# Optimization experiments

Hardware: AMD Instinct MI355X
Metric: run time of the kernel (lower is better)

## Reference

```python
import jax, jax.numpy as jnp
import numpy as np

HIDDEN = 4096
N_HEADS = 32
N_KV_HEADS = 8
HEAD_DIM = 128
N_GROUPS = N_HEADS // N_KV_HEADS
ROPE_THETA = 10000.0
QMAX = 127.0
B, S = 1, 2048


def setup_inputs() -> dict:
    key = jax.random.key(0)
    ks = jax.random.split(key, 5)
    hidden_states = jax.random.normal(ks[0], (B, S, HIDDEN), dtype=jnp.float32)
    # additive causal mask (Llama style: 0 on/below diagonal, large negative above)
    tril = jnp.tril(jnp.ones((S, S), dtype=bool))
    attention_mask = jnp.where(tril, 0.0, -1e9).astype(jnp.float32)[None, None]
    position_ids = jnp.arange(S, dtype=jnp.int64 if jax.config.jax_enable_x64 else jnp.int32)[None].astype(jnp.int32)
    sc = 1.0 / np.sqrt(HIDDEN)
    wq = jax.random.normal(ks[1], (HIDDEN, N_HEADS * HEAD_DIM), dtype=jnp.float32) * sc
    wk = jax.random.normal(ks[2], (HIDDEN, N_KV_HEADS * HEAD_DIM), dtype=jnp.float32) * sc
    wv = jax.random.normal(ks[3], (HIDDEN, N_KV_HEADS * HEAD_DIM), dtype=jnp.float32) * sc
    wo = jax.random.normal(ks[4], (N_HEADS * HEAD_DIM, HIDDEN), dtype=jnp.float32) * sc
    return {"hidden_states": hidden_states, "attention_mask": attention_mask,
            "position_ids": position_ids, "wq": wq, "wk": wk, "wv": wv, "wo": wo}


def _rope_cos_sin(position_ids):
    # [B, S, HEAD_DIM]
    inv_freq = 1.0 / (ROPE_THETA ** (jnp.arange(0, HEAD_DIM, 2, dtype=jnp.float32) / HEAD_DIM))
    freqs = position_ids.astype(jnp.float32)[..., None] * inv_freq  # [B,S,HEAD_DIM//2]
    emb = jnp.concatenate([freqs, freqs], axis=-1)
    return jnp.cos(emb), jnp.sin(emb)


def _rotate_half(x):
    x1, x2 = jnp.split(x, 2, axis=-1)
    return jnp.concatenate([-x2, x1], axis=-1)


def _fake_quant(x):
    scale = jnp.max(jnp.abs(x)) / QMAX  # global absmax
    return jnp.round(x / scale) * scale


def reference(hidden_states, attention_mask, position_ids, wq, wk, wv, wo):
    bsz, q_len, _ = hidden_states.shape
    q = (hidden_states @ wq).reshape(bsz, q_len, N_HEADS, HEAD_DIM).transpose(0, 2, 1, 3)
    k = (hidden_states @ wk).reshape(bsz, q_len, N_KV_HEADS, HEAD_DIM).transpose(0, 2, 1, 3)
    v = (hidden_states @ wv).reshape(bsz, q_len, N_KV_HEADS, HEAD_DIM).transpose(0, 2, 1, 3)

    cos, sin = _rope_cos_sin(position_ids)  # [B,S,D]
    cos, sin = cos[:, None], sin[:, None]   # broadcast over heads
    q = q * cos + _rotate_half(q) * sin
    k = k * cos + _rotate_half(k) * sin

    # repeat_kv: [B, Hkv, S, D] -> [B, H, S, D]
    k = jnp.repeat(k, N_GROUPS, axis=1)
    v = jnp.repeat(v, N_GROUPS, axis=1)

    # fake quant: global absmax round-trip on Q, K, V
    q = _fake_quant(q)
    k = _fake_quant(k)
    v = _fake_quant(v)

    scores = jnp.einsum('bhqd,bhkd->bhqk', q, k) / np.sqrt(HEAD_DIM)
    scores = scores + attention_mask
    probs = jax.nn.softmax(scores.astype(jnp.float32), axis=-1).astype(q.dtype)
    attn = jnp.einsum('bhqk,bhkd->bhqd', probs, v)
    attn = attn.transpose(0, 2, 1, 3).reshape(bsz, q_len, N_HEADS * HEAD_DIM)
    return attn @ wo
```

## Files before the change

kernel.cpp:

```cpp
#include <hip/hip_runtime.h>
#include <math.h>

#define S_LEN 2048
#define HID 4096
#define NH 32
#define NKV 8
#define HD 128
#define NQKV 6144

typedef __bf16 bf16x8 __attribute__((ext_vector_type(8)));
typedef float f32x4 __attribute__((ext_vector_type(4)));
typedef short short8v __attribute__((ext_vector_type(8)));

__device__ inline short f2bf(float f) {
  union { float f; unsigned u; } a; a.f = f;
  unsigned r = a.u + 0x7fffu + ((a.u >> 16) & 1u);
  return (short)(r >> 16);
}

__device__ inline void glds16(const void* g, void* l) {
  __builtin_amdgcn_global_load_lds((const __attribute__((address_space(1))) void*)g,
                                   (__attribute__((address_space(3))) void*)l, 16, 0, 0);
}

template <int CTRL>
__device__ inline float dpp_max_step(float x) {
  int y = __builtin_amdgcn_update_dpp(0, __float_as_int(x), CTRL, 0xf, 0xf, false);
  return fmaxf(x, __int_as_float(y));
}

__global__ __launch_bounds__(256) void cast_h(const float* __restrict__ X,
                                              short* __restrict__ Y, int n4) {
  int i = blockIdx.x * 256 + threadIdx.x;
  if (i >= n4) return;
  float4 v = ((const float4*)X)[i];
  short4 o;
  o.x = f2bf(v.x); o.y = f2bf(v.y); o.z = f2bf(v.z); o.w = f2bf(v.w);
  ((short4*)Y)[i] = o;
}

__global__ __launch_bounds__(256) void cast_wt(const float* __restrict__ W,
                                               short* __restrict__ Wt, int Ncols) {
  __shared__ float t[32][33];
  int n0 = blockIdx.x * 32, k0 = blockIdx.y * 32;
  int tx = threadIdx.x, ty = threadIdx.y;
  for (int j = 0; j < 4; j++)
    t[ty + 8 * j][tx] = W[(size_t)(k0 + ty + 8 * j) * Ncols + n0 + tx];
  __syncthreads();
  for (int j = 0; j < 4; j++)
    Wt[(size_t)(n0 + ty + 8 * j) * 4096 + k0 + tx] = f2bf(t[tx][ty + 8 * j]);
}

__global__ void rope_table(const int* __restrict__ pos_ids, float* __restrict__ tc,
                           float* __restrict__ ts) {
  int p = blockIdx.x, i = threadIdx.x;
  float pos = (float)pos_ids[p];
  float inv = powf(10000.0f, -((float)(2 * i)) * (1.0f / 128.0f));
  float a = pos * inv;
  tc[p * 64 + i] = cosf(a);
  ts[p * 64 + i] = sinf(a);
}

__global__ __launch_bounds__(256) void rope_absmax(float* __restrict__ C,
                                                   const float* __restrict__ tc,
                                                   const float* __restrict__ ts,
                                                   unsigned* __restrict__ scal) {
  __shared__ float lc[64], lsn[64];
  __shared__ float red[3][4];
  const int p = blockIdx.x, t = threadIdx.x;
  if (t < 64) { lc[t] = tc[p * 64 + t]; lsn[t] = ts[p * 64 + t]; }
  __syncthreads();
  float* row = C + (size_t)p * NQKV;
  float mq = 0.f, mk = 0.f, mv = 0.f;
#pragma unroll
  for (int j = 0; j < 8; j++) {
    int idx = t + 256 * j;
    int i = idx & 63, col = (idx >> 6) * 128 + i;
    float c = lc[i], s = lsn[i];
    float x1 = row[col], x2 = row[col + 64];
    float y1 = x1 * c - x2 * s, y2 = x2 * c + x1 * s;
    row[col] = y1; row[col + 64] = y2;
    mq = fmaxf(mq, fmaxf(fabsf(y1), fabsf(y2)));
  }
#pragma unroll
  for (int j = 0; j < 2; j++) {
    int idx = t + 256 * j;
    int i = idx & 63, col = 4096 + (idx >> 6) * 128 + i;
    float c = lc[i], s = lsn[i];
    float x1 = row[col], x2 = row[col + 64];
    float y1 = x1 * c - x2 * s, y2 = x2 * c + x1 * s;
    row[col] = y1; row[col + 64] = y2;
    mk = fmaxf(mk, fmaxf(fabsf(y1), fabsf(y2)));
  }
#pragma unroll
  for (int j = 0; j < 4; j++) {
    float v = row[5120 + t + 256 * j];
    mv = fmaxf(mv, fabsf(v));
  }
  for (int off = 32; off; off >>= 1) {
    mq = fmaxf(mq, __shfl_xor(mq, off, 64));
    mk = fmaxf(mk, __shfl_xor(mk, off, 64));
    mv = fmaxf(mv, __shfl_xor(mv, off, 64));
  }
  const int wave = t >> 6;
  if ((t & 63) == 0) { red[0][wave] = mq; red[1][wave] = mk; red[2][wave] = mv; }
  __syncthreads();
  if (t < 3) {
    float m = fmaxf(fmaxf(red[t][0], red[t][1]), fmaxf(red[t][2], red[t][3]));
    atomicMax(scal + t, __float_as_uint(m));
  }
}

__global__ __launch_bounds__(256) void quant_q(const float* __restrict__ C,
                                               const unsigned* __restrict__ scal,
                                               short* __restrict__ Qi) {
  int idx = blockIdx.x * 256 + threadIdx.x;
  float scale = __uint_as_float(scal[0]) * (1.0f / 127.0f);
  int p = idx >> 12, c = idx & 4095;
  Qi[idx] = f2bf(rintf(C[(size_t)p * NQKV + c] / scale));
}

__global__ __launch_bounds__(256) void quant_k(const float* __restrict__ C,
                                               const unsigned* __restrict__ scal,
                                               short* __restrict__ Ki) {
  int idx = blockIdx.x * 256 + threadIdx.x;
  float scale = __uint_as_float(scal[1]) * (1.0f / 127.0f);
  int h = idx >> 18, p = (idx >> 7) & 2047, d = idx & 127;
  Ki[idx] = f2bf(rintf(C[(size_t)p * NQKV + 4096 + h * 128 + d] / scale));
}

__global__ __launch_bounds__(256) void quant_vt(const float* __restrict__ C,
                                                const unsigned* __restrict__ scal,
                                                short* __restrict__ Vt) {
  __shared__ float t[64][65];
  int h = blockIdx.x, pt = blockIdx.y, dt = blockIdx.z;
  float scale = __uint_as_float(scal[2]) * (1.0f / 127.0f);
  int tid = threadIdx.x;
  for (int j = 0; j < 16; j++) {
    int q = tid + 256 * j;
    int pl = q >> 6, dl = q & 63;
    t[dl][pl] = C[(size_t)(pt * 64 + pl) * NQKV + 5120 + h * 128 + dt * 64 + dl];
  }
  __syncthreads();
  for (int j = 0; j < 16; j++) {
    int q = tid + 256 * j;
    int dl = q >> 6, pl = q & 63;
    Vt[(size_t)(h * 128 + dt * 64 + dl) * 2048 + pt * 64 + pl] =
        f2bf(rintf(t[dl][pl] / scale));
  }
}

__global__ __launch_bounds__(256, 2) void gemm_bt(const short* __restrict__ A, int lda,
                                                  const short* __restrict__ B,
                                                  float* __restrict__ C, int ldc, int K) {
  __shared__ alignas(16) short As[2][4096];
  __shared__ alignas(16) short Bs[2][4096];
  const int tid = threadIdx.x;
  const int wave = tid >> 6, lane = tid & 63;
  const int quad = lane >> 4, l15 = lane & 15;
  const int m0 = blockIdx.y * 128, n0 = blockIdx.x * 128;
  const int wm = (wave >> 1) * 64, wn = (wave & 1) * 64;
  f32x4 acc[4][4] = {};
  const int sr = wave * 16 + (lane >> 2);
  const int sg = (lane & 3) * 8;
  const short* Ag0 = A + (size_t)(m0 + sr) * lda + sg;
  const short* Ag1 = A + (size_t)(m0 + 64 + sr) * lda + sg;
  const short* Bg0 = B + (size_t)(n0 + sr) * K + sg;
  const short* Bg1 = B + (size_t)(n0 + 64 + sr) * K + sg;
  auto stage = [&](int kk, int b) {
    glds16(Ag0 + kk, &As[b][wave * 512]);
    glds16(Ag1 + kk, &As[b][2048 + wave * 512]);
    glds16(Bg0 + kk, &Bs[b][wave * 512]);
    glds16(Bg1 + kk, &Bs[b][2048 + wave * 512]);
  };
  stage(0, 0);
  int b = 0;
  for (int k0 = 0; k0 < K; k0 += 32) {
    __syncthreads();
    const int nk = (k0 + 32 < K) ? k0 + 32 : k0;
    stage(nk, b ^ 1);
    bf16x8 af[4], bfr[4];
#pragma unroll
    for (int t = 0; t < 4; t++) {
      af[t] = *(const bf16x8*)&As[b][(wm + t * 16 + l15) * 32 + quad * 8];
      bfr[t] = *(const bf16x8*)&Bs[b][(wn + t * 16 + l15) * 32 + quad * 8];
    }
#pragma unroll
    for (int tm = 0; tm < 4; tm++)
#pragma unroll
      for (int tn = 0; tn < 4; tn++)
        acc[tm][tn] =
            __builtin_amdgcn_mfma_f32_16x16x32_bf16(af[tm], bfr[tn], acc[tm][tn], 0, 0, 0);
    b ^= 1;
  }
#pragma unroll
  for (int tm = 0; tm < 4; tm++)
#pragma unroll
    for (int tn = 0; tn < 4; tn++) {
      const int row = m0 + wm + tm * 16 + quad * 4;
      const int col = n0 + wn + tn * 16 + l15;
#pragma unroll
      for (int r = 0; r < 4; r++) C[(size_t)(row + r) * ldc + col] = acc[tm][tn][r];
    }
}

__global__ __launch_bounds__(512, 2) void gemm_bt8(const short* __restrict__ A, int lda,
                                                   const short* __restrict__ B, int ldb,
                                                   float* __restrict__ C, int ldc, int K) {
  __shared__ alignas(16) short As[2][16384];
  __shared__ alignas(16) short Bs[2][16384];
  const int tid = threadIdx.x;
  const int wave = tid >> 6, lane = tid & 63;
  const int quad = lane >> 4, l15 = lane & 15;
  const int wm = wave >> 2, wn = wave & 3;
  const int m0 = blockIdx.y * 256, n0 = blockIdx.x * 256;

  const int rsub = lane >> 3;
  const int csw = (lane & 7) ^ rsub;
  size_t asrc[4], bsrc[4];
#pragma unroll
  for (int s = 0; s < 4; s++) {
    int row = s * 64 + wave * 8 + rsub;
    asrc[s] = (size_t)(m0 + row) * lda + csw * 8;
    bsrc[s] = (size_t)(n0 + row) * ldb + csw * 8;
  }
  const int nt = K >> 6;

  auto stA = [&](int t2) {
    const int kk = (t2 < nt ? t2 : nt - 1) << 6;
#pragma unroll
    for (int s = 0; s < 4; s++)
      glds16(A + asrc[s] + kk, &As[t2 & 1][(s * 64 + wave * 8) * 64]);
  };
  auto stB = [&](int t2) {
    const int kk = (t2 < nt ? t2 : nt - 1) << 6;
#pragma unroll
    for (int s = 0; s < 4; s++)
      glds16(B + bsrc[s] + kk, &Bs[t2 & 1][(s * 64 + wave * 8) * 64]);
  };

  int swq[2];
#pragma unroll
  for (int kc = 0; kc < 2; kc++)
    swq[kc] = l15 * 64 + (((kc * 4 + quad) ^ (l15 & 7)) * 8);

  f32x4 acc[8][4] = {};

  stB(0); stA(0);
  stB(1);
  asm volatile("s_waitcnt vmcnt(4)" ::: "memory");
  __builtin_amdgcn_s_barrier();

  for (int t = 0; t < nt; t++) {
    const short* Ab = As[t & 1];
    const short* Bb = Bs[t & 1];
    stA(t + 1);
    bf16x8 bfr[4][2];
#pragma unroll
    for (int n = 0; n < 4; n++) {
      bfr[n][0] = *(const bf16x8*)&Bb[(wn * 64 + n * 16) * 64 + swq[0]];
      bfr[n][1] = *(const bf16x8*)&Bb[(wn * 64 + n * 16) * 64 + swq[1]];
    }
    asm volatile("s_waitcnt lgkmcnt(0)" ::: "memory");
    __builtin_amdgcn_sched_barrier(0);
    __builtin_amdgcn_s_barrier();
    stB(t + 2);
    __builtin_amdgcn_s_setprio(1);
#pragma unroll
    for (int m = 0; m < 8; m++) {
      bf16x8 a0 = *(const bf16x8*)&Ab[(wm * 128 + m * 16) * 64 + swq[0]];
      bf16x8 a1 = *(const bf16x8*)&Ab[(wm * 128 + m * 16) * 64 + swq[1]];
#pragma unroll
      for (int n = 0; n < 4; n++) {
        acc[m][n] = __builtin_amdgcn_mfma_f32_16x16x32_bf16(a0, bfr[n][0], acc[m][n], 0, 0, 0);
        acc[m][n] = __builtin_amdgcn_mfma_f32_16x16x32_bf16(a1, bfr[n][1], acc[m][n], 0, 0, 0);
      }
    }
    __builtin_amdgcn_s_setprio(0);
    asm volatile("s_waitcnt vmcnt(4)" ::: "memory");
    __builtin_amdgcn_s_barrier();
    __builtin_amdgcn_sched_barrier(0);
  }
#pragma unroll
  for (int m = 0; m < 8; m++)
#pragma unroll
    for (int n = 0; n < 4; n++) {
      const int row = m0 + wm * 128 + m * 16 + quad * 4;
      const int col = n0 + wn * 64 + n * 16 + l15;
#pragma unroll
      for (int r = 0; r < 4; r++) C[(size_t)(row + r) * ldc + col] = acc[m][n][r];
    }
}

__global__ __launch_bounds__(256, 2) void attn_fused(const short* __restrict__ Qi,
                                                     const short* __restrict__ Ki,
                                                     const short* __restrict__ Vt,
                                                     const unsigned* __restrict__ scal,
                                                     short* __restrict__ Oa) {
  __shared__ alignas(16) short Ks[2][64 * 128];
  __shared__ alignas(16) short Vs[2][128 * 64];
  __shared__ alignas(16) short Ps[4][16 * 72];
  const int tid = threadIdx.x;
  const int wave = tid >> 6, lane = tid & 63;
  const int quad = lane >> 4, l15 = lane & 15;
  const int swz = l15 & 7;
  const int h = blockIdx.x & 31, pq = blockIdx.x >> 5;
  const int kvh = h >> 2;
  const float qs = __uint_as_float(scal[0]) * (1.0f / 127.0f);
  const float ksc = __uint_as_float(scal[1]) * (1.0f / 127.0f);
  const float vsc = __uint_as_float(scal[2]) * (1.0f / 127.0f);
  const float sscale = qs * ksc * 0.08838834764831845f * 1.4426950408889634f;
  const short* Kg = Ki + (size_t)kvh * S_LEN * HD;
  const short* Vg = Vt + (size_t)kvh * HD * S_LEN;

  union { short8v s; bf16x8 b; } uone;
  uone.s = short8v{0x3F80, 0x3F80, 0x3F80, 0x3F80, 0x3F80, 0x3F80, 0x3F80, 0x3F80};
  const bf16x8 vone = uone.b;

  int koff[4], voff[4];
#pragma unroll
  for (int j = 0; j < 4; j++) {
    int slot = j * 256 + tid;
    int r = slot >> 4, seg = slot & 15;
    koff[j] = r * 128 + ((seg ^ (r & 7)) * 8);
    int vr = slot >> 3, vseg = slot & 7;
    voff[j] = vr * 2048 + ((vseg ^ (vr & 7)) * 8);
  }
  auto stage = [&](int k0, int b) {
#pragma unroll
    for (int j = 0; j < 4; j++)
      glds16(Kg + (size_t)k0 * HD + koff[j], &Ks[b][(j * 256 + wave * 64) * 8]);
#pragma unroll
    for (int j = 0; j < 4; j++)
      glds16(Vg + (size_t)k0 + voff[j], &Vs[b][(j * 256 + wave * 64) * 8]);
  };

  stage(0, 0);
  int buf = 0;
  for (int ph = 0; ph < 2; ph++) {
    const int qt = ph ? 31 - pq : pq;
    const int rw = qt * 64 + wave * 16;
    bf16x8 aq[4];
#pragma unroll
    for (int kc = 0; kc < 4; kc++)
      aq[kc] = *(const bf16x8*)(Qi + (size_t)(rw + l15) * 4096 + h * 128 + kc * 32 +
                                quad * 8);
    f32x4 o[9] = {};
    float m_[4] = {-INFINITY, -INFINITY, -INFINITY, -INFINITY};
    const int nkt = qt + 1;
    for (int kt = 0; kt < nkt; kt++) {
      const int k0 = kt * 64;
      __syncthreads();
      const int nx = (kt + 1 < nkt) ? k0 + 64 : 0;
      stage(nx, buf ^ 1);

      const short* Kb = Ks[buf];
      const short* Vb = Vs[buf];
      f32x4 sf[4];
      __builtin_amdgcn_s_setprio(1);
#pragma unroll
      for (int tn = 0; tn < 4; tn++) {
        f32x4 s = {0.f, 0.f, 0.f, 0.f};
#pragma unroll
        for (int kc = 0; kc < 4; kc++) {
          bf16x8 bk = *(const bf16x8*)&Kb[(tn * 16 + l15) * 128 + ((kc * 4 + quad) ^ swz) * 8];
          s = __builtin_amdgcn_mfma_f32_16x16x32_bf16(aq[kc], bk, s, 0, 0, 0);
        }
        sf[tn] = s;
      }
      __builtin_amdgcn_s_setprio(0);

      const bool diag = (kt == qt);
#pragma unroll
      for (int r = 0; r < 4; r++) {
        const int grow = rw + quad * 4 + r;
        float mx = -3.0e38f;
        if (diag) {
#pragma unroll
          for (int tn = 0; tn < 4; tn++) {
            float v = sf[tn][r] * sscale;
            if (k0 + tn * 16 + l15 > grow) v = -3.0e38f;
            sf[tn][r] = v;
            mx = fmaxf(mx, v);
          }
        } else {
#pragma unroll
          for (int tn = 0; tn < 4; tn++) {
            float v = sf[tn][r] * sscale;
            sf[tn][r] = v;
            mx = fmaxf(mx, v);
          }
        }
        mx = dpp_max_step<0x121>(mx);
        mx = dpp_max_step<0x122>(mx);
        mx = dpp_max_step<0x124>(mx);
        mx = dpp_max_step<0x128>(mx);
        const float mo = m_[r];
        const float mn = fmaxf(mo, mx);
        m_[r] = mn;
        const float alpha = __builtin_amdgcn_exp2f(mo - mn);
#pragma unroll
        for (int tn = 0; tn < 4; tn++) {
          float p = __builtin_amdgcn_exp2f(sf[tn][r] - mn);
          Ps[wave][(quad * 4 + r) * 72 + tn * 16 + l15] =
              (short)((__float_as_uint(p) + 0x8000u) >> 16);
        }
        if (__ballot(alpha != 1.0f)) {
#pragma unroll
          for (int t = 0; t < 9; t++) o[t][r] *= alpha;
        }
      }
      __builtin_amdgcn_s_setprio(1);
#pragma unroll
      for (int kk = 0; kk < 2; kk++) {
        bf16x8 ap = *(const bf16x8*)&Ps[wave][l15 * 72 + kk * 32 + quad * 8];
#pragma unroll
        for (int tn = 0; tn < 8; tn++) {
          bf16x8 bv = *(const bf16x8*)&Vb[(tn * 16 + l15) * 64 + ((kk * 4 + quad) ^ swz) * 8];
          o[tn] = __builtin_amdgcn_mfma_f32_16x16x32_bf16(ap, bv, o[tn], 0, 0, 0);
        }
        o[8] = __builtin_amdgcn_mfma_f32_16x16x32_bf16(ap, vone, o[8], 0, 0, 0);
      }
      __builtin_amdgcn_s_setprio(0);
      buf ^= 1;
    }
#pragma unroll
    for (int r = 0; r < 4; r++) {
      const int grow = rw + quad * 4 + r;
      const float sc = vsc / o[8][r];
#pragma unroll
      for (int tn = 0; tn < 8; tn++)
        Oa[(size_t)grow * 4096 + h * 128 + tn * 16 + l15] = f2bf(o[tn][r] * sc);
    }
  }
}

extern "C" void kernel_launch(void* const* d_in, const int* in_sizes, int n_in,
                              void* d_out, int out_size, void* d_ws, size_t ws_size,
                              hipStream_t stream) {
  (void)in_sizes; (void)n_in; (void)out_size; (void)ws_size;
  const float* H  = (const float*)d_in[0];
  const int*   pos = (const int*)d_in[2];
  const float* wq = (const float*)d_in[3];
  const float* wk = (const float*)d_in[4];
  const float* wv = (const float*)d_in[5];
  const float* wo = (const float*)d_in[6];
  char* ws = (char*)d_ws;
  short* Hb   = (short*)(ws + 0);
  short* Wt   = (short*)(ws + 16777216);
  short* Wot  = (short*)(ws + 67108864);
  float* C    = (float*)(ws + 100663296);
  short* Qi   = (short*)(ws + 150994944);
  short* Ki   = (short*)(ws + 167772160);
  short* Vt   = (short*)(ws + 171966464);
  short* Oa   = (short*)(ws + 176160768);
  float* tc   = (float*)(ws + 192937984);
  float* tsn  = (float*)(ws + 193462272);
  unsigned* scal = (unsigned*)(ws + 193986560);

  hipLaunchKernelGGL(cast_h, dim3(8192), dim3(256), 0, stream, H, Hb, 2097152);
  hipLaunchKernelGGL(cast_wt, dim3(128, 128), dim3(32, 8), 0, stream, wq, Wt, 4096);
  hipLaunchKernelGGL(cast_wt, dim3(32, 128), dim3(32, 8), 0, stream, wk,
                     Wt + (size_t)4096 * 4096, 1024);
  hipLaunchKernelGGL(cast_wt, dim3(32, 128), dim3(32, 8), 0, stream, wv,
                     Wt + (size_t)5120 * 4096, 1024);
  hipLaunchKernelGGL(cast_wt, dim3(128, 128), dim3(32, 8), 0, stream, wo, Wot, 4096);
  hipLaunchKernelGGL(rope_table, dim3(2048), dim3(64), 0, stream, pos, tc, tsn);
  hipMemsetAsync(scal, 0, 16, stream);
  hipLaunchKernelGGL(gemm_bt8, dim3(24, 8), dim3(512), 0, stream, Hb, 4096, Wt, 4096, C,
                     6144, 4096);
  hipLaunchKernelGGL(rope_absmax, dim3(2048), dim3(256), 0, stream, C, tc, tsn, scal);
  hipLaunchKernelGGL(quant_q, dim3(32768), dim3(256), 0, stream, C, scal, Qi);
  hipLaunchKernelGGL(quant_k, dim3(8192), dim3(256), 0, stream, C, scal, Ki);
  hipLaunchKernelGGL(quant_vt, dim3(8, 32, 2), dim3(256), 0, stream, C, scal, Vt);
  hipLaunchKernelGGL(attn_fused, dim3(512), dim3(256), 0, stream, Qi, Ki, Vt, scal, Oa);
  hipLaunchKernelGGL(gemm_bt, dim3(32, 16), dim3(256), 0, stream, Oa, 4096, Wot,
                     (float*)d_out, 4096, 4096);
}
```

Baseline: 596.7 us.

## Interleave GEMM tile loads with MFMA quarters in a finer-grained pipeline

Restructures the 256x256 bf16 GEMM main loop so each K-step is split into four quarters: each quarter loads part of the A fragments from LDS, issues half of an A or B global-to-LDS prefetch, and runs a quarter of the MFMAs, with barriers in between. The aim is to spread global loads and LDS reads across the compute phase instead of issuing them in bursts. It also removes the s_setprio calls around the MFMA blocks in the attention kernel. The extra barriers per step and the changed lgkmcnt and vmcnt accounting may add synchronisation overhead or introduce hazards.

```diff
diff --git a/kernel.cpp b/kernel.cpp
--- a/kernel.cpp
+++ b/kernel.cpp
@@ -217,26 +217,28 @@
 
   const int rsub = lane >> 3;
   const int csw = (lane & 7) ^ rsub;
-  size_t asrc[4], bsrc[4];
-#pragma unroll
-  for (int s = 0; s < 4; s++) {
-    int row = s * 64 + wave * 8 + rsub;
-    asrc[s] = (size_t)(m0 + row) * lda + csw * 8;
-    bsrc[s] = (size_t)(n0 + row) * ldb + csw * 8;
-  }
+  size_t asrc[2][2], bsrc[2][2];
+#pragma unroll
+  for (int h = 0; h < 2; h++)
+#pragma unroll
+    for (int g = 0; g < 2; g++) {
+      int row = h * 128 + g * 64 + wave * 8 + rsub;
+      asrc[h][g] = (size_t)(m0 + row) * lda + csw * 8;
+      bsrc[h][g] = (size_t)(n0 + row) * ldb + csw * 8;
+    }
   const int nt = K >> 6;
 
-  auto stA = [&](int t2) {
-    const int kk = (t2 < nt ? t2 : nt - 1) << 6;
-#pragma unroll
-    for (int s = 0; s < 4; s++)
-      glds16(A + asrc[s] + kk, &As[t2 & 1][(s * 64 + wave * 8) * 64]);
-  };
-  auto stB = [&](int t2) {
-    const int kk = (t2 < nt ? t2 : nt - 1) << 6;
-#pragma unroll
-    for (int s = 0; s < 4; s++)
-      glds16(B + bsrc[s] + kk, &Bs[t2 & 1][(s * 64 + wave * 8) * 64]);
+  auto stH = [&](int tau, int isB, int h) {
+    const int kk = (tau < nt ? tau : nt - 1) << 6;
+    if (isB) {
+#pragma unroll
+      for (int g = 0; g < 2; g++)
+        glds16(B + bsrc[h][g] + kk, &Bs[tau & 1][(h * 128 + g * 64 + wave * 8) * 64]);
+    } else {
+#pragma unroll
+      for (int g = 0; g < 2; g++)
+        glds16(A + asrc[h][g] + kk, &As[tau & 1][(h * 128 + g * 64 + wave * 8) * 64]);
+    }
   };
 
   int swq[2];
@@ -246,40 +248,68 @@
 
   f32x4 acc[8][4] = {};
 
-  stB(0); stA(0);
-  stB(1);
+  auto ldA = [&](const short* Ab, int q, bf16x8* a) {
+    a[0] = *(const bf16x8*)&Ab[(wm * 128 + (2 * q) * 16) * 64 + swq[0]];
+    a[1] = *(const bf16x8*)&Ab[(wm * 128 + (2 * q) * 16) * 64 + swq[1]];
+    a[2] = *(const bf16x8*)&Ab[(wm * 128 + (2 * q + 1) * 16) * 64 + swq[0]];
+    a[3] = *(const bf16x8*)&Ab[(wm * 128 + (2 * q + 1) * 16) * 64 + swq[1]];
+  };
+  auto mfmaQ = [&](int q, bf16x8* a, bf16x8 (&bfr)[4][2]) {
+    __builtin_amdgcn_s_setprio(1);
+#pragma unroll
+    for (int n = 0; n < 4; n++) {
+      acc[2 * q][n] = __builtin_amdgcn_mfma_f32_16x16x32_bf16(a[0], bfr[n][0], acc[2 * q][n], 0, 0, 0);
+      acc[2 * q][n] = __builtin_amdgcn_mfma_f32_16x16x32_bf16(a[1], bfr[n][1], acc[2 * q][n], 0, 0, 0);
+      acc[2 * q + 1][n] = __builtin_amdgcn_mfma_f32_16x16x32_bf16(a[2], bfr[n][0], acc[2 * q + 1][n], 0, 0, 0);
+      acc[2 * q + 1][n] = __builtin_amdgcn_mfma_f32_16x16x32_bf16(a[3], bfr[n][1], acc[2 * q + 1][n], 0, 0, 0);
+    }
+    __builtin_amdgcn_s_setprio(0);
+  };
+
+  stH(0, 1, 0); stH(0, 1, 1); stH(0, 0, 0); stH(0, 0, 1);
+  stH(1, 1, 0); stH(1, 1, 1);
   asm volatile("s_waitcnt vmcnt(4)" ::: "memory");
   __builtin_amdgcn_s_barrier();
 
-  for (int t = 0; t < nt; t++) {
-    const short* Ab = As[t & 1];
-    const short* Bb = Bs[t & 1];
-    stA(t + 1);
-    bf16x8 bfr[4][2];
-#pragma unroll
-    for (int n = 0; n < 4; n++) {
-      bfr[n][0] = *(const bf16x8*)&Bb[(wn * 64 + n * 16) * 64 + swq[0]];
-      bfr[n][1] = *(const bf16x8*)&Bb[(wn * 64 + n * 16) * 64 + swq[1]];
-    }
-    asm volatile("s_waitcnt lgkmcnt(0)" ::: "memory");
-    __builtin_amdgcn_sched_barrier(0);
-    __builtin_amdgcn_s_barrier();
-    stB(t + 2);
-    __builtin_amdgcn_s_setprio(1);
-#pragma unroll
-    for (int m = 0; m < 8; m++) {
-      bf16x8 a0 = *(const bf16x8*)&Ab[(wm * 128 + m * 16) * 64 + swq[0]];
-      bf16x8 a1 = *(const bf16x8*)&Ab[(wm * 128 + m * 16) * 64 + swq[1]];
+  for (int t2 = 0; t2 < nt; t2 += 2) {
+#pragma unroll
+    for (int half = 0; half < 2; half++) {
+      const int tau = t2 + half;
+      const short* Ab = As[tau & 1];
+      const short* Bb = Bs[tau & 1];
+      bf16x8 bfr[4][2], a[4];
 #pragma unroll
       for (int n = 0; n < 4; n++) {
-        acc[m][n] = __builtin_amdgcn_mfma_f32_16x16x32_bf16(a0, bfr[n][0], acc[m][n], 0, 0, 0);
-        acc[m][n] = __builtin_amdgcn_mfma_f32_16x16x32_bf16(a1, bfr[n][1], acc[m][n], 0, 0, 0);
+        bfr[n][0] = *(const bf16x8*)&Bb[(wn * 64 + n * 16) * 64 + swq[0]];
+        bfr[n][1] = *(const bf16x8*)&Bb[(wn * 64 + n * 16) * 64 + swq[1]];
       }
-    }
-    __builtin_amdgcn_s_setprio(0);
-    asm volatile("s_waitcnt vmcnt(4)" ::: "memory");
-    __builtin_amdgcn_s_barrier();
-    __builtin_amdgcn_sched_barrier(0);
+      ldA(Ab, 0, a);
+      stH(tau + 1, 0, 0);
+      asm volatile("s_waitcnt lgkmcnt(8)" ::: "memory");
+      __builtin_amdgcn_s_barrier();
+      asm volatile("s_waitcnt lgkmcnt(0)" ::: "memory");
+      mfmaQ(0, a, bfr);
+      __builtin_amdgcn_s_barrier();
+      ldA(Ab, 1, a);
+      stH(tau + 1, 0, 1);
+      __builtin_amdgcn_s_barrier();
+      asm volatile("s_waitcnt lgkmcnt(0)" ::: "memory");
+      mfmaQ(1, a, bfr);
+      __builtin_amdgcn_s_barrier();
+      ldA(Ab, 2, a);
+      stH(tau + 2, 1, 0);
+      __builtin_amdgcn_s_barrier();
+      asm volatile("s_waitcnt lgkmcnt(0)" ::: "memory");
+      mfmaQ(2, a, bfr);
+      __builtin_amdgcn_s_barrier();
+      ldA(Ab, 3, a);
+      stH(tau + 2, 1, 1);
+      __builtin_amdgcn_s_barrier();
+      asm volatile("s_waitcnt lgkmcnt(0)" ::: "memory");
+      mfmaQ(3, a, bfr);
+      asm volatile("s_waitcnt vmcnt(4)" ::: "memory");
+      __builtin_amdgcn_s_barrier();
+    }
   }
 #pragma unroll
   for (int m = 0; m < 8; m++)
@@ -357,7 +387,6 @@
       const short* Kb = Ks[buf];
       const short* Vb = Vs[buf];
       f32x4 sf[4];
-      __builtin_amdgcn_s_setprio(1);
 #pragma unroll
       for (int tn = 0; tn < 4; tn++) {
         f32x4 s = {0.f, 0.f, 0.f, 0.f};
@@ -368,7 +397,6 @@
         }
         sf[tn] = s;
       }
-      __builtin_amdgcn_s_setprio(0);
 
       const bool diag = (kt == qt);
 #pragma unroll
@@ -410,7 +438,6 @@
           for (int t = 0; t < 9; t++) o[t][r] *= alpha;
         }
       }
-      __builtin_amdgcn_s_setprio(1);
 #pragma unroll
       for (int kk = 0; kk < 2; kk++) {
         bf16x8 ap = *(const bf16x8*)&Ps[wave][l15 * 72 + kk * 32 + quad * 8];
@@ -421,7 +448,6 @@
         }
         o[8] = __builtin_amdgcn_mfma_f32_16x16x32_bf16(ap, vone, o[8], 0, 0, 0);
       }
-      __builtin_amdgcn_s_setprio(0);
       buf ^= 1;
     }
 #pragma unroll
```

New measurement: 567.6 us. 1.05x faster.

## Retile QKV GEMM to 256x192 blocks with interleaved LDS loads and MFMA

Applied to the files above, without the earlier changes.

The QKV projection GEMM moves from 256x256 to 256x192 output tiles, so the grid grows from 24x8=192 to 32x8=256 blocks, better matching the CU count. The K-loop is split into four quarter-phases, each interleaving A-fragment LDS reads, global-to-LDS prefetch issue and MFMA work, with finer vmcnt waits and extra barriers. B fragments for the next tile are loaded at the end of each iteration. Separately, the s_setprio hints are removed from the attention kernel. The smaller tiles reduce per-block reuse, and the added barriers cost some sync overhead.

```diff
diff --git a/kernel.cpp b/kernel.cpp
--- a/kernel.cpp
+++ b/kernel.cpp
@@ -208,35 +208,31 @@
                                                    const short* __restrict__ B, int ldb,
                                                    float* __restrict__ C, int ldc, int K) {
   __shared__ alignas(16) short As[2][16384];
-  __shared__ alignas(16) short Bs[2][16384];
+  __shared__ alignas(16) short Bs[2][12288];
   const int tid = threadIdx.x;
   const int wave = tid >> 6, lane = tid & 63;
   const int quad = lane >> 4, l15 = lane & 15;
   const int wm = wave >> 2, wn = wave & 3;
-  const int m0 = blockIdx.y * 256, n0 = blockIdx.x * 256;
+  const int m0 = blockIdx.y * 256, n0 = blockIdx.x * 192;
 
   const int rsub = lane >> 3;
   const int csw = (lane & 7) ^ rsub;
-  size_t asrc[4], bsrc[4];
-#pragma unroll
-  for (int s = 0; s < 4; s++) {
-    int row = s * 64 + wave * 8 + rsub;
-    asrc[s] = (size_t)(m0 + row) * lda + csw * 8;
-    bsrc[s] = (size_t)(n0 + row) * ldb + csw * 8;
-  }
+  size_t asrc[4], bsrc[3];
+#pragma unroll
+  for (int c = 0; c < 4; c++)
+    asrc[c] = (size_t)(m0 + c * 64 + wave * 8 + rsub) * lda + csw * 8;
+#pragma unroll
+  for (int c = 0; c < 3; c++)
+    bsrc[c] = (size_t)(n0 + c * 64 + wave * 8 + rsub) * ldb + csw * 8;
   const int nt = K >> 6;
 
-  auto stA = [&](int t2) {
-    const int kk = (t2 < nt ? t2 : nt - 1) << 6;
-#pragma unroll
-    for (int s = 0; s < 4; s++)
-      glds16(A + asrc[s] + kk, &As[t2 & 1][(s * 64 + wave * 8) * 64]);
-  };
-  auto stB = [&](int t2) {
-    const int kk = (t2 < nt ? t2 : nt - 1) << 6;
-#pragma unroll
-    for (int s = 0; s < 4; s++)
-      glds16(B + bsrc[s] + kk, &Bs[t2 & 1][(s * 64 + wave * 8) * 64]);
+  auto stA = [&](int tau, int c) {
+    const int kk = (tau < nt ? tau : nt - 1) << 6;
+    glds16(A + asrc[c] + kk, &As[tau & 1][(c * 64 + wave * 8) * 64]);
+  };
+  auto stB = [&](int tau, int c) {
+    const int kk = (tau < nt ? tau : nt - 1) << 6;
+    glds16(B + bsrc[c] + kk, &Bs[tau & 1][(c * 64 + wave * 8) * 64]);
   };
 
   int swq[2];
@@ -244,49 +240,70 @@
   for (int kc = 0; kc < 2; kc++)
     swq[kc] = l15 * 64 + (((kc * 4 + quad) ^ (l15 & 7)) * 8);
 
-  f32x4 acc[8][4] = {};
-
-  stB(0); stA(0);
-  stB(1);
-  asm volatile("s_waitcnt vmcnt(4)" ::: "memory");
+  f32x4 acc[8][3] = {};
+
+  auto ldA = [&](const short* Ab, int q, bf16x8* a) {
+    a[0] = *(const bf16x8*)&Ab[(wm * 128 + (2 * q) * 16) * 64 + swq[0]];
+    a[1] = *(const bf16x8*)&Ab[(wm * 128 + (2 * q) * 16) * 64 + swq[1]];
+    a[2] = *(const bf16x8*)&Ab[(wm * 128 + (2 * q + 1) * 16) * 64 + swq[0]];
+    a[3] = *(const bf16x8*)&Ab[(wm * 128 + (2 * q + 1) * 16) * 64 + swq[1]];
+  };
+  auto ldB = [&](const short* Bb, bf16x8 (&b)[3][2]) {
+#pragma unroll
+    for (int n = 0; n < 3; n++) {
+      b[n][0] = *(const bf16x8*)&Bb[(wn * 48 + n * 16) * 64 + swq[0]];
+      b[n][1] = *(const bf16x8*)&Bb[(wn * 48 + n * 16) * 64 + swq[1]];
+    }
+  };
+  auto mfmaQ = [&](int q, bf16x8* a, bf16x8 (&b)[3][2]) {
+    __builtin_amdgcn_s_setprio(1);
+#pragma unroll
+    for (int n = 0; n < 3; n++) {
+      acc[2 * q][n] = __builtin_amdgcn_mfma_f32_16x16x32_bf16(a[0], b[n][0], acc[2 * q][n], 0, 0, 0);
+      acc[2 * q][n] = __builtin_amdgcn_mfma_f32_16x16x32_bf16(a[1], b[n][1], acc[2 * q][n], 0, 0, 0);
+      acc[2 * q + 1][n] = __builtin_amdgcn_mfma_f32_16x16x32_bf16(a[2], b[n][0], acc[2 * q + 1][n], 0, 0, 0);
+      acc[2 * q + 1][n] = __builtin_amdgcn_mfma_f32_16x16x32_bf16(a[3], b[n][1], acc[2 * q + 1][n], 0, 0, 0);
+    }
+    __builtin_amdgcn_s_setprio(0);
+  };
+
+  stB(0, 0); stB(0, 1); stB(0, 2);
+  stA(0, 0); stA(0, 1); stA(0, 2); stA(0, 3);
+  stB(1, 0); stB(1, 1); stB(1, 2);
+  asm volatile("s_waitcnt vmcnt(3)" ::: "memory");
   __builtin_amdgcn_s_barrier();
+
+  bf16x8 bfr[3][2], acur[4], anext[4];
+  ldB(Bs[0], bfr);
 
   for (int t = 0; t < nt; t++) {
     const short* Ab = As[t & 1];
-    const short* Bb = Bs[t & 1];
-    stA(t + 1);
-    bf16x8 bfr[4][2];
-#pragma unroll
-    for (int n = 0; n < 4; n++) {
-      bfr[n][0] = *(const bf16x8*)&Bb[(wn * 64 + n * 16) * 64 + swq[0]];
-      bfr[n][1] = *(const bf16x8*)&Bb[(wn * 64 + n * 16) * 64 + swq[1]];
-    }
-    asm volatile("s_waitcnt lgkmcnt(0)" ::: "memory");
-    __builtin_amdgcn_sched_barrier(0);
+    ldA(Ab, 0, acur);
+    ldA(Ab, 1, anext);
+    stA(t + 1, 0); stA(t + 1, 1);
+    mfmaQ(0, acur, bfr);
     __builtin_amdgcn_s_barrier();
-    stB(t + 2);
-    __builtin_amdgcn_s_setprio(1);
-#pragma unroll
-    for (int m = 0; m < 8; m++) {
-      bf16x8 a0 = *(const bf16x8*)&Ab[(wm * 128 + m * 16) * 64 + swq[0]];
-      bf16x8 a1 = *(const bf16x8*)&Ab[(wm * 128 + m * 16) * 64 + swq[1]];
-#pragma unroll
-      for (int n = 0; n < 4; n++) {
-        acc[m][n] = __builtin_amdgcn_mfma_f32_16x16x32_bf16(a0, bfr[n][0], acc[m][n], 0, 0, 0);
-        acc[m][n] = __builtin_amdgcn_mfma_f32_16x16x32_bf16(a1, bfr[n][1], acc[m][n], 0, 0, 0);
-      }
-    }
-    __builtin_amdgcn_s_setprio(0);
-    asm volatile("s_waitcnt vmcnt(4)" ::: "memory");
+    ldA(Ab, 2, acur);
+    stA(t + 1, 2); stA(t + 1, 3);
+    mfmaQ(1, anext, bfr);
     __builtin_amdgcn_s_barrier();
-    __builtin_amdgcn_sched_barrier(0);
+    ldA(Ab, 3, anext);
+    stB(t + 2, 0); stB(t + 2, 1);
+    mfmaQ(2, acur, bfr);
+    asm volatile("s_waitcnt vmcnt(6)" ::: "memory");
+    __builtin_amdgcn_s_barrier();
+    stB(t + 2, 2);
+    mfmaQ(3, anext, bfr);
+    ldB(Bs[(t + 1) & 1], bfr);
+    asm volatile("s_waitcnt vmcnt(3)" ::: "memory");
+    __builtin_amdgcn_s_barrier();
   }
 #pragma unroll
   for (int m = 0; m < 8; m++)
 #pragma unroll
-    for (int n = 0; n < 4; n++) {
+    for (int n = 0; n < 3; n++) {
       const int row = m0 + wm * 128 + m * 16 + quad * 4;
-      const int col = n0 + wn * 64 + n * 16 + l15;
+      const int col = n0 + wn * 48 + n * 16 + l15;
 #pragma unroll
       for (int r = 0; r < 4; r++) C[(size_t)(row + r) * ldc + col] = acc[m][n][r];
     }
@@ -357,7 +374,6 @@
       const short* Kb = Ks[buf];
       const short* Vb = Vs[buf];
       f32x4 sf[4];
-      __builtin_amdgcn_s_setprio(1);
 #pragma unroll
       for (int tn = 0; tn < 4; tn++) {
         f32x4 s = {0.f, 0.f, 0.f, 0.f};
@@ -368,7 +384,6 @@
         }
         sf[tn] = s;
       }
-      __builtin_amdgcn_s_setprio(0);
 
       const bool diag = (kt == qt);
 #pragma unroll
@@ -410,7 +425,6 @@
           for (int t = 0; t < 9; t++) o[t][r] *= alpha;
         }
       }
-      __builtin_amdgcn_s_setprio(1);
 #pragma unroll
       for (int kk = 0; kk < 2; kk++) {
         bf16x8 ap = *(const bf16x8*)&Ps[wave][l15 * 72 + kk * 32 + quad * 8];
@@ -421,7 +435,6 @@
         }
         o[8] = __builtin_amdgcn_mfma_f32_16x16x32_bf16(ap, vone, o[8], 0, 0, 0);
       }
-      __builtin_amdgcn_s_setprio(0);
       buf ^= 1;
     }
 #pragma unroll
@@ -467,7 +480,7 @@
   hipLaunchKernelGGL(cast_wt, dim3(128, 128), dim3(32, 8), 0, stream, wo, Wot, 4096);
   hipLaunchKernelGGL(rope_table, dim3(2048), dim3(64), 0, stream, pos, tc, tsn);
   hipMemsetAsync(scal, 0, 16, stream);
-  hipLaunchKernelGGL(gemm_bt8, dim3(24, 8), dim3(512), 0, stream, Hb, 4096, Wt, 4096, C,
+  hipLaunchKernelGGL(gemm_bt8, dim3(32, 8), dim3(512), 0, stream, Hb, 4096, Wt, 4096, C,
                      6144, 4096);
   hipLaunchKernelGGL(rope_absmax, dim3(2048), dim3(256), 0, stream, C, tc, tsn, scal);
   hipLaunchKernelGGL(quant_q, dim3(32768), dim3(256), 0, stream, C, scal, Qi);
```

Measured after the change: 575.5 us. 1.04x faster.
